# Optimization experiments

Hardware: AMD Instinct MI355X
Metric: run time of the kernel (lower is better)

The kernel has to match this reference:

```python
import jax, jax.numpy as jnp
import numpy as np

EPS = 1e-07
NUM_ITERATIONS = 3

B, O, H, W, I, D = 8, 32, 14, 14, 32, 16


def squash(s, axis=-1):
    # squared norm over capsule dim
    sq = jnp.sum(s * s, axis=axis)                      # [..., ] norms
    safe = jnp.sqrt(sq + EPS)
    factor = sq / (1.0 + sq)
    return (factor / safe)[..., None] * s


def setup_inputs() -> dict:
    key = jax.random.key(0)
    k1, = jax.random.split(key, 1)
    preds = jax.random.normal(k1, (B, O, H, W, I, D), dtype=jnp.float32)
    b = jnp.zeros((1, O, H, W, I), dtype=jnp.float32)   # routing logits param
    return {"tensor_of_prediction_vector": preds, "b": b}


def reference(tensor_of_prediction_vector, b):
    preds = tensor_of_prediction_vector                 # [B,O,H,W,I,D]
    c = jax.nn.softmax(b, axis=-1)                      # [1,O,H,W,I]
    v = squash(jnp.sum(c[..., None] * preds, axis=-2))  # [B,O,H,W,D]
    b_batch = b
    for _ in range(NUM_ITERATIONS):
        # agreement: dot(pred, v) over capsule dim -> [B,O,H,W,I]
        b_batch = b_batch + jnp.sum(preds * v[..., None, :], axis=-1)
        c = jax.nn.softmax(b_batch, axis=-1)
        v = squash(jnp.sum(preds * c[..., None], axis=-2))
    return v
```

## Files before the change

### kernel.cpp

```cpp
#include <hip/hip_runtime.h>


#define EPSQ 1e-7f
#define LOG2E 1.442695041f

constexpr int OHW   = 6272;
constexpr int SITES = 50176;
constexpr int THREADS = 256;
constexpr int BLOCKS  = SITES / 32;

__device__ __forceinline__ float dpp1(float x) {
    return __int_as_float(__builtin_amdgcn_mov_dpp(__float_as_int(x), 0xB1, 0xF, 0xF, true));
}
__device__ __forceinline__ float dpp2(float x) {
    return __int_as_float(__builtin_amdgcn_mov_dpp(__float_as_int(x), 0x4E, 0xF, 0xF, true));
}
__device__ __forceinline__ float dpp4(float x) {
    return __int_as_float(__builtin_amdgcn_mov_dpp(__float_as_int(x), 0x141, 0xF, 0xF, true));
}
__device__ __forceinline__ void fma4(float4& a, float c, const float4& x) {
    a.x = fmaf(c, x.x, a.x); a.y = fmaf(c, x.y, a.y);
    a.z = fmaf(c, x.z, a.z); a.w = fmaf(c, x.w, a.w);
}
__device__ __forceinline__ float dot4(const float4& a, const float4& b) {
    return fmaf(a.x, b.x, fmaf(a.y, b.y, fmaf(a.z, b.z, a.w * b.w)));
}
__device__ __forceinline__ void red8_4(float4& a) {
    a.x += dpp1(a.x); a.y += dpp1(a.y); a.z += dpp1(a.z); a.w += dpp1(a.w);
    a.x += dpp2(a.x); a.y += dpp2(a.y); a.z += dpp2(a.z); a.w += dpp2(a.w);
    a.x += dpp4(a.x); a.y += dpp4(a.y); a.z += dpp4(a.z); a.w += dpp4(a.w);
}

__device__ __forceinline__ void gload16(const char* g, float4* l) {
    __builtin_amdgcn_global_load_lds(
        (const __attribute__((address_space(1))) void*)g,
        (__attribute__((address_space(3))) void*)l, 16, 0, 0);
}

__global__ __launch_bounds__(256, 4) void routing_kernel(
    const float* __restrict__ preds,
    const float* __restrict__ bparam,
    float* __restrict__ out)
{
    __shared__ float4 lds4[2048];
    const int tid  = threadIdx.x;
    const int lane = tid & 63;
    const int wib  = tid >> 6;
    const int wave = blockIdx.x * 4 + wib;
    const int g    = lane & 7;
    const int s_w  = lane >> 3;
    const int site = wave * 8 + s_w;

    float4* bufA = lds4 + wib * 512;
    float4* bufB = bufA + 256;
    const char* pgc = (const char*)((const float4*)preds + (size_t)wave * 1024);

    const int sohw = site % OHW;
    const float* bs = bparam + (size_t)sohw * 32 + g;
    float bl[4];
    #pragma unroll
    for (int k = 0; k < 4; ++k) bl[k] = bs[8 * k];
    asm volatile("" ::: "memory");

    const int hi  = lane >> 5;
    const int w32 = lane & 31;
    int vofs[4];
    #pragma unroll
    for (int t = 0; t < 4; ++t) {
        const int x = 2 * t + hi;
        vofs[t] = (x * 128 + (w32 ^ x)) * 16;
    }

    #pragma unroll
    for (int t = 0; t < 4; ++t) gload16(pgc + vofs[t], bufA + t * 64);
    #pragma unroll
    for (int t = 0; t < 4; ++t) gload16(pgc + vofs[t] + 512, bufB + t * 64);

    float4 p[4][4];
    const int rbase = s_w * 32;
    const int rkey  = s_w;

    auto read_ph = [&](int k, const float4* buf) {
        #pragma unroll
        for (int u = 0; u < 4; ++u)
            p[k][u] = buf[rbase + ((4 * g + u) ^ rkey)];
    };

    asm volatile("s_waitcnt vmcnt(4)" ::: "memory");
    read_ph(0, bufA);
    asm volatile("s_waitcnt lgkmcnt(0)" ::: "memory");
    #pragma unroll
    for (int t = 0; t < 4; ++t) gload16(pgc + vofs[t] + 1024, bufA + t * 64);

    asm volatile("s_waitcnt vmcnt(4)" ::: "memory");
    read_ph(1, bufB);
    asm volatile("s_waitcnt lgkmcnt(0)" ::: "memory");
    #pragma unroll
    for (int t = 0; t < 4; ++t) gload16(pgc + vofs[t] + 1536, bufB + t * 64);

    asm volatile("s_waitcnt vmcnt(4)" ::: "memory");
    read_ph(2, bufA);
    asm volatile("s_waitcnt vmcnt(0)" ::: "memory");
    read_ph(3, bufB);

    #pragma unroll
    for (int k = 0; k < 4; ++k) bl[k] *= LOG2E;

    float4 s0, s1, s2, s3;
    float  f;

    auto pass = [&]() {
        float sm = 0.0f;
        s0 = make_float4(0,0,0,0); s1 = make_float4(0,0,0,0);
        s2 = make_float4(0,0,0,0); s3 = make_float4(0,0,0,0);
        #pragma unroll
        for (int k = 0; k < 4; ++k) {
            const float e = __builtin_amdgcn_exp2f(bl[k]);
            sm += e;
            fma4(s0, e, p[k][0]); fma4(s1, e, p[k][1]);
            fma4(s2, e, p[k][2]); fma4(s3, e, p[k][3]);
        }
        sm += dpp1(sm);
        sm += dpp2(sm);
        sm += dpp4(sm);
        const float r = __frcp_rn(sm);
        red8_4(s0); red8_4(s1); red8_4(s2); red8_4(s3);

        const float sqt = dot4(s0, s0) + dot4(s1, s1) + dot4(s2, s2) + dot4(s3, s3);
        const float sq  = r * r * sqt;
        f = sq * __frcp_rn(1.0f + sq) * __frsqrt_rn(sq + EPSQ) * r;
    };

    pass();

    #pragma unroll
    for (int it = 0; it < 3; ++it) {
        const float fl = f * LOG2E;
        #pragma unroll
        for (int k = 0; k < 4; ++k) {
            const float qk = dot4(p[k][0], s0) + dot4(p[k][1], s1)
                           + dot4(p[k][2], s2) + dot4(p[k][3], s3);
            bl[k] = fmaf(fl, qk, bl[k]);
        }
        pass();
    }

    if (g < 4) {
        float4 wv = (g == 0) ? s0 : (g == 1) ? s1 : (g == 2) ? s2 : s3;
        wv.x *= f; wv.y *= f; wv.z *= f; wv.w *= f;
        ((float4*)out)[(size_t)site * 4 + g] = wv;
    }
}

extern "C" void kernel_launch(void* const* d_in, const int* in_sizes, int n_in,
                              void* d_out, int out_size, void* d_ws, size_t ws_size,
                              hipStream_t stream) {
    const float* preds  = (const float*)d_in[0];
    const float* bparam = (const float*)d_in[1];
    float* out = (float*)d_out;
    routing_kernel<<<BLOCKS, THREADS, 0, stream>>>(preds, bparam, out);
}
```

Measured before the change: 28.39 us.

## Process two site groups per wave, overlapping second group's loads with first's routing

Each wave now handles 16 sites instead of 8, launching half as many blocks. While routing iterations for the first group of 8 sites run, the global-to-LDS loads for the second group are issued and staged, so memory latency is hidden behind compute. Launch bounds drop to 2 blocks per CU to allow the doubled register footprint of two prediction tiles. This adds register pressure and fewer resident waves, which may reduce latency hiding from occupancy.

```diff
diff --git a/kernel.cpp b/kernel.cpp
--- a/kernel.cpp
+++ b/kernel.cpp
@@ -7,7 +7,7 @@
 constexpr int OHW   = 6272;
 constexpr int SITES = 50176;
 constexpr int THREADS = 256;
-constexpr int BLOCKS  = SITES / 32;
+constexpr int BLOCKS  = SITES / 64;
 
 __device__ __forceinline__ float dpp1(float x) {
     return __int_as_float(__builtin_amdgcn_mov_dpp(__float_as_int(x), 0xB1, 0xF, 0xF, true));
@@ -37,7 +37,12 @@
         (__attribute__((address_space(3))) void*)l, 16, 0, 0);
 }
 
-__global__ __launch_bounds__(256, 4) void routing_kernel(
+#define VMCNT4 asm volatile("s_waitcnt vmcnt(4)" ::: "memory")
+#define VMCNT0 asm volatile("s_waitcnt vmcnt(0)" ::: "memory")
+#define LGKM0  asm volatile("s_waitcnt lgkmcnt(0)" ::: "memory")
+#define SBAR   __builtin_amdgcn_sched_barrier(0)
+
+__global__ __launch_bounds__(256, 2) void routing_kernel(
     const float* __restrict__ preds,
     const float* __restrict__ bparam,
     float* __restrict__ out)
@@ -49,18 +54,19 @@
     const int wave = blockIdx.x * 4 + wib;
     const int g    = lane & 7;
     const int s_w  = lane >> 3;
-    const int site = wave * 8 + s_w;
+    const int siteA = wave * 16 + s_w;
+    const int siteB = siteA + 8;
 
-    float4* bufA = lds4 + wib * 512;
-    float4* bufB = bufA + 256;
-    const char* pgc = (const char*)((const float4*)preds + (size_t)wave * 1024);
+    float4* slot0 = lds4 + wib * 512;
+    float4* slot1 = slot0 + 256;
+    const char* pgA = (const char*)((const float4*)preds + (size_t)wave * 2048);
+    const char* pgB = pgA + 16384;
 
-    const int sohw = site % OHW;
-    const float* bs = bparam + (size_t)sohw * 32 + g;
-    float bl[4];
+    const float* bsA = bparam + (size_t)(siteA % OHW) * 32 + g;
+    const float* bsB = bparam + (size_t)(siteB % OHW) * 32 + g;
+    float blA[4], blB[4];
     #pragma unroll
-    for (int k = 0; k < 4; ++k) bl[k] = bs[8 * k];
-    asm volatile("" ::: "memory");
+    for (int k = 0; k < 4; ++k) { blA[k] = bsA[8 * k]; blB[k] = bsB[8 * k]; }
 
     const int hi  = lane >> 5;
     const int w32 = lane & 31;
@@ -72,44 +78,43 @@
     }
 
     #pragma unroll
-    for (int t = 0; t < 4; ++t) gload16(pgc + vofs[t], bufA + t * 64);
+    for (int t = 0; t < 4; ++t) gload16(pgA + vofs[t], slot0 + t * 64);
     #pragma unroll
-    for (int t = 0; t < 4; ++t) gload16(pgc + vofs[t] + 512, bufB + t * 64);
+    for (int t = 0; t < 4; ++t) gload16(pgA + vofs[t] + 512, slot1 + t * 64);
 
-    float4 p[4][4];
+    #pragma unroll
+    for (int k = 0; k < 4; ++k) { blA[k] *= LOG2E; blB[k] *= LOG2E; }
+
+    float4 pA[4][4], pB[4][4];
     const int rbase = s_w * 32;
-    const int rkey  = s_w;
 
-    auto read_ph = [&](int k, const float4* buf) {
+    auto read_ph = [&](float4 (&p)[4][4], int k, const float4* buf) {
         #pragma unroll
         for (int u = 0; u < 4; ++u)
-            p[k][u] = buf[rbase + ((4 * g + u) ^ rkey)];
+            p[k][u] = buf[rbase + ((4 * g + u) ^ s_w)];
     };
 
-    asm volatile("s_waitcnt vmcnt(4)" ::: "memory");
-    read_ph(0, bufA);
-    asm volatile("s_waitcnt lgkmcnt(0)" ::: "memory");
+    VMCNT4; read_ph(pA, 0, slot0); LGKM0;
     #pragma unroll
-    for (int t = 0; t < 4; ++t) gload16(pgc + vofs[t] + 1024, bufA + t * 64);
-
-    asm volatile("s_waitcnt vmcnt(4)" ::: "memory");
-    read_ph(1, bufB);
-    asm volatile("s_waitcnt lgkmcnt(0)" ::: "memory");
+    for (int t = 0; t < 4; ++t) gload16(pgA + vofs[t] + 1024, slot0 + t * 64);
+    SBAR;
+    VMCNT4; read_ph(pA, 1, slot1); LGKM0;
     #pragma unroll
-    for (int t = 0; t < 4; ++t) gload16(pgc + vofs[t] + 1536, bufB + t * 64);
-
-    asm volatile("s_waitcnt vmcnt(4)" ::: "memory");
-    read_ph(2, bufA);
-    asm volatile("s_waitcnt vmcnt(0)" ::: "memory");
-    read_ph(3, bufB);
-
+    for (int t = 0; t < 4; ++t) gload16(pgA + vofs[t] + 1536, slot1 + t * 64);
+    SBAR;
+    VMCNT4; read_ph(pA, 2, slot0); LGKM0;
     #pragma unroll
-    for (int k = 0; k < 4; ++k) bl[k] *= LOG2E;
+    for (int t = 0; t < 4; ++t) gload16(pgB + vofs[t], slot0 + t * 64);
+    SBAR;
+    VMCNT4; read_ph(pA, 3, slot1); LGKM0;
+    #pragma unroll
+    for (int t = 0; t < 4; ++t) gload16(pgB + vofs[t] + 512, slot1 + t * 64);
+    SBAR;
 
     float4 s0, s1, s2, s3;
     float  f;
 
-    auto pass = [&]() {
+    auto pass = [&](float4 (&p)[4][4], float (&bl)[4]) {
         float sm = 0.0f;
         s0 = make_float4(0,0,0,0); s1 = make_float4(0,0,0,0);
         s2 = make_float4(0,0,0,0); s3 = make_float4(0,0,0,0);
@@ -120,21 +125,14 @@
             fma4(s0, e, p[k][0]); fma4(s1, e, p[k][1]);
             fma4(s2, e, p[k][2]); fma4(s3, e, p[k][3]);
         }
-        sm += dpp1(sm);
-        sm += dpp2(sm);
-        sm += dpp4(sm);
+        sm += dpp1(sm); sm += dpp2(sm); sm += dpp4(sm);
         const float r = __frcp_rn(sm);
         red8_4(s0); red8_4(s1); red8_4(s2); red8_4(s3);
-
         const float sqt = dot4(s0, s0) + dot4(s1, s1) + dot4(s2, s2) + dot4(s3, s3);
         const float sq  = r * r * sqt;
         f = sq * __frcp_rn(1.0f + sq) * __frsqrt_rn(sq + EPSQ) * r;
     };
-
-    pass();
-
-    #pragma unroll
-    for (int it = 0; it < 3; ++it) {
+    auto agree = [&](float4 (&p)[4][4], float (&bl)[4]) {
         const float fl = f * LOG2E;
         #pragma unroll
         for (int k = 0; k < 4; ++k) {
@@ -142,13 +140,46 @@
                            + dot4(p[k][2], s2) + dot4(p[k][3], s3);
             bl[k] = fmaf(fl, qk, bl[k]);
         }
-        pass();
+    };
+
+    pass(pA, blA);
+    agree(pA, blA);
+    VMCNT4; read_ph(pB, 0, slot0); LGKM0;
+    #pragma unroll
+    for (int t = 0; t < 4; ++t) gload16(pgB + vofs[t] + 1024, slot0 + t * 64);
+    SBAR;
+    pass(pA, blA);
+    agree(pA, blA);
+    VMCNT4; read_ph(pB, 1, slot1); LGKM0;
+    #pragma unroll
+    for (int t = 0; t < 4; ++t) gload16(pgB + vofs[t] + 1536, slot1 + t * 64);
+    SBAR;
+    pass(pA, blA);
+    agree(pA, blA);
+    VMCNT4; read_ph(pB, 2, slot0);
+    SBAR;
+    pass(pA, blA);
+
+    if (g < 4) {
+        float4 wv = (g == 0) ? s0 : (g == 1) ? s1 : (g == 2) ? s2 : s3;
+        wv.x *= f; wv.y *= f; wv.z *= f; wv.w *= f;
+        ((float4*)out)[(size_t)siteA * 4 + g] = wv;
+    }
+
+    VMCNT0; read_ph(pB, 3, slot1);
+    SBAR;
+
+    pass(pB, blB);
+    #pragma unroll
+    for (int it = 0; it < 3; ++it) {
+        agree(pB, blB);
+        pass(pB, blB);
     }
 
     if (g < 4) {
         float4 wv = (g == 0) ? s0 : (g == 1) ? s1 : (g == 2) ? s2 : s3;
         wv.x *= f; wv.y *= f; wv.z *= f; wv.w *= f;
-        ((float4*)out)[(size_t)site * 4 + g] = wv;
+        ((float4*)out)[(size_t)siteB * 4 + g] = wv;
     }
 }
 
```

After: 28.50 us. Within noise of the previous version (+0.4%).
